# Optimization experiments

Measured on AMD Instinct MI355X. Metric: run time of the kernel, lower is better.

## Reference

```python
import jax, jax.numpy as jnp
import numpy as np

D_MODEL = 1024
NUM_HEADS = 16
HEAD_DIM = D_MODEL // NUM_HEADS
SEQ_LEN = 2048
BATCH = 2


def setup_inputs() -> dict:
    key = jax.random.key(0)
    ks = jax.random.split(key, 8)
    s = 1.0 / np.sqrt(D_MODEL)
    x = jax.random.normal(ks[0], (BATCH, SEQ_LEN, D_MODEL), jnp.float32)
    Wq = jax.random.normal(ks[1], (D_MODEL, D_MODEL), jnp.float32) * s
    Wk = jax.random.normal(ks[2], (D_MODEL, D_MODEL), jnp.float32) * s
    Wv = jax.random.normal(ks[3], (D_MODEL, D_MODEL), jnp.float32) * s
    Wo = jax.random.normal(ks[4], (D_MODEL, D_MODEL), jnp.float32) * s
    bq = jnp.zeros((D_MODEL,), jnp.float32)
    bk = jnp.zeros((D_MODEL,), jnp.float32)
    bv = jnp.zeros((D_MODEL,), jnp.float32)
    bo = jnp.zeros((D_MODEL,), jnp.float32)
    pos_embed = jax.random.normal(ks[5], (SEQ_LEN, HEAD_DIM), jnp.float32) * (1.0 / np.sqrt(HEAD_DIM))
    alpha = jnp.ones((NUM_HEADS, 1, 1), jnp.float32)
    beta = jnp.zeros((NUM_HEADS, 1, 1), jnp.float32)
    mask = jnp.ones((BATCH, SEQ_LEN), jnp.int32)
    return {"x": x, "mask": mask, "Wq": Wq, "bq": bq, "Wk": Wk, "bk": bk,
            "Wv": Wv, "bv": bv, "Wo": Wo, "bo": bo,
            "pos_embed": pos_embed, "alpha": alpha, "beta": beta}


def reference(x, mask, Wq, bq, Wk, bk, Wv, bv, Wo, bo, pos_embed, alpha, beta):
    B, S, _ = x.shape
    H, Dh = NUM_HEADS, HEAD_DIM
    # projections (torch Linear: x @ W^T + b), reshape to [B,H,S,Dh]
    def proj(W, b):
        return (x @ W.T + b).reshape(B, S, H, Dh).transpose(0, 2, 1, 3)
    q = proj(Wq, bq)
    k = proj(Wk, bk)
    v = proj(Wv, bv)
    # content scores [B,H,S,S]
    content = jnp.einsum('bhqd,bhkd->bhqk', q, k) / np.sqrt(Dh).astype(np.float32)
    # position scores [S,S] -> broadcast; combined with per-head alpha/beta
    pe = pos_embed[:S]
    pos_attn = pe @ pe.T  # [S,S]
    scores = content + (alpha * pos_attn[None] + beta)[None]  # [B,H,S,S]
    # mask: [B,S] broadcast over heads and query positions (key-side mask)
    scores = jnp.where(mask[:, None, None, :] == 0, -jnp.inf, scores)
    probs = jax.nn.softmax(scores, axis=-1)
    out = jnp.einsum('bhqk,bhkd->bhqd', probs, v)  # [B,H,S,Dh]
    out = out.transpose(0, 2, 1, 3).reshape(B, S, H * Dh)
    return out @ Wo.T + bo
```

## Files before the change

kernel.cpp:

```cpp
#include <hip/hip_runtime.h>

#define BATCH 2
#define SEQ   2048
#define NH    16
#define DH    64
#define DA    128
#define DM    1024
#define MTOT  (BATCH*SEQ)

typedef _Float16 f16x8 __attribute__((ext_vector_type(8)));
typedef _Float16 f16x4 __attribute__((ext_vector_type(4)));
typedef float    f32x4 __attribute__((ext_vector_type(4)));
typedef float    f32x16 __attribute__((ext_vector_type(16)));

#define LOG2E 1.44269504088896340736f

#define OFF_X16 0u
#define OFF_WQ  8388608u
#define OFF_WK  10485760u
#define OFF_WV  12582912u
#define OFF_WO  14680064u
#define OFF_QA  16777216u
#define OFF_KA  33554432u
#define OFF_VT  50331648u
#define OFF_AO  58720256u

__device__ __forceinline__ void gload_lds16(const _Float16* g, _Float16* l) {
  __builtin_amdgcn_global_load_lds(
      (const __attribute__((address_space(1))) unsigned int*)g,
      (__attribute__((address_space(3))) unsigned int*)l, 16, 0, 0);
}

__device__ __forceinline__ float fexp2(float x) {
  float r;
  asm("v_exp_f32 %0, %1" : "=v"(r) : "v"(x));
  return r;
}

__device__ __forceinline__ unsigned pk2(float a, float b) {
  auto v = __builtin_amdgcn_cvt_pkrtz(a, b);
  return *(unsigned*)&v;
}

__global__ __launch_bounds__(256) void prep(
    const float* __restrict__ x,  const float* __restrict__ wq,
    const float* __restrict__ wk, const float* __restrict__ wv,
    const float* __restrict__ wo, _Float16* __restrict__ dst,
    const float* __restrict__ pe, const float* __restrict__ alpha,
    _Float16* __restrict__ Qa, _Float16* __restrict__ Ka)
{
  int bid = blockIdx.x;
  if (bid < 4096) {
    int i = bid * 256 + threadIdx.x;
    const float* src;
    if (i < 524288) {
      src = x + (size_t)i * 8;
    } else {
      int j = i - 524288;
      int wi = j >> 17;
      const float* w = (wi == 0) ? wq : ((wi == 1) ? wk : ((wi == 2) ? wv : wo));
      src = w + (size_t)(j & 131071) * 8;
    }
    float4 a = ((const float4*)src)[0];
    float4 c = ((const float4*)src)[1];
    f16x8 hv;
    hv[0]=(_Float16)a.x; hv[1]=(_Float16)a.y; hv[2]=(_Float16)a.z; hv[3]=(_Float16)a.w;
    hv[4]=(_Float16)c.x; hv[5]=(_Float16)c.y; hv[6]=(_Float16)c.z; hv[7]=(_Float16)c.w;
    *(f16x8*)(dst + (size_t)i * 8) = hv;
  } else {
    int idx = (bid - 4096) * 256 + threadIdx.x;
    int c8 = idx & 7;
    int s  = (idx >> 3) & 2047;
    int h  = (idx >> 14) & 15;
    int b  = idx >> 18;
    const float4* p4 = (const float4*)(pe + s * 64 + c8 * 8);
    float4 a = p4[0], c = p4[1];
    float al = alpha[h] * LOG2E;
    f16x8 hk, hq;
    hk[0]=(_Float16)a.x; hk[1]=(_Float16)a.y; hk[2]=(_Float16)a.z; hk[3]=(_Float16)a.w;
    hk[4]=(_Float16)c.x; hk[5]=(_Float16)c.y; hk[6]=(_Float16)c.z; hk[7]=(_Float16)c.w;
    hq[0]=(_Float16)(al*a.x); hq[1]=(_Float16)(al*a.y); hq[2]=(_Float16)(al*a.z); hq[3]=(_Float16)(al*a.w);
    hq[4]=(_Float16)(al*c.x); hq[5]=(_Float16)(al*c.y); hq[6]=(_Float16)(al*c.z); hq[7]=(_Float16)(al*c.w);
    size_t o = ((size_t)((b * NH + h) * SEQ + s)) * DA + 64 + c8 * 8;
    *(f16x8*)&Qa[o] = hq;
    *(f16x8*)&Ka[o] = hk;
  }
}

template<int MODE>
__global__ __launch_bounds__(512) void gemm_nt(
    const _Float16* __restrict__ A,
    const _Float16* __restrict__ W0, const _Float16* __restrict__ W1,
    const _Float16* __restrict__ W2,
    const float* __restrict__ b0, const float* __restrict__ b1,
    const float* __restrict__ b2,
    _Float16* __restrict__ Qa, _Float16* __restrict__ Ka,
    _Float16* __restrict__ Vt, float* __restrict__ Out)
{
  __shared__ _Float16 As[128 * 64];
  __shared__ _Float16 Bs[128 * 64];
  const int tid = threadIdx.x;
  const int w = tid >> 6, lane = tid & 63;
  const int g = lane >> 4, l16 = lane & 15;
  const int wm = w >> 2, wn = w & 3;

  int lin = blockIdx.x;
  int xcd = lin & 7, j = lin >> 3;
  int mblk, nb_all;
  if (MODE == 0) { mblk = (xcd & 3) * 8 + (j & 7); nb_all = (xcd >> 2) * 12 + (j >> 3); }
  else           { mblk = xcd * 4 + (j & 3);       nb_all = j >> 2; }

  const _Float16* Bp; const float* biasp;
  int which = 0, nblk = nb_all;
  if (MODE == 0) {
    which = nb_all >> 3; nblk = nb_all & 7;
    Bp = (which == 0) ? W0 : ((which == 1) ? W1 : W2);
    biasp = (which == 0) ? b0 : ((which == 1) ? b1 : b2);
  } else {
    Bp = W0; biasp = b0;
  }

  f32x4 zero4 = {0.f, 0.f, 0.f, 0.f};
  f32x4 acc[4][2];
  #pragma unroll
  for (int mb = 0; mb < 4; ++mb)
    #pragma unroll
    for (int nb = 0; nb < 2; ++nb) acc[mb][nb] = zero4;

  const _Float16* Abase = A  + (size_t)mblk * 128 * DM;
  const _Float16* Bbase = Bp + (size_t)nblk * 128 * DM;

  for (int kt = 0; kt < DM / 64; ++kt) {
    __syncthreads();
    #pragma unroll
    for (int ii = 0; ii < 2; ++ii) {
      int i = w * 2 + ii;
      int rt = i * 8 + (lane >> 3);
      int cg = (lane & 7) ^ (rt & 7);
      gload_lds16(Abase + (size_t)rt * DM + kt * 64 + cg * 8, &As[i * 512]);
    }
    #pragma unroll
    for (int ii = 0; ii < 2; ++ii) {
      int i = w * 2 + ii;
      int rt = i * 8 + (lane >> 3);
      int cg = (lane & 7) ^ (rt & 7);
      gload_lds16(Bbase + (size_t)rt * DM + kt * 64 + cg * 8, &Bs[i * 512]);
    }
    __syncthreads();
    #pragma unroll
    for (int ks = 0; ks < 2; ++ks) {
      f16x8 av[4], bv[2];
      #pragma unroll
      for (int mb = 0; mb < 4; ++mb) {
        int rt = wm * 64 + mb * 16 + l16;
        av[mb] = *(const f16x8*)&As[rt * 64 + (((ks * 4 + g) ^ (rt & 7)) * 8)];
      }
      #pragma unroll
      for (int nb = 0; nb < 2; ++nb) {
        int rt = wn * 32 + nb * 16 + l16;
        bv[nb] = *(const f16x8*)&Bs[rt * 64 + (((ks * 4 + g) ^ (rt & 7)) * 8)];
      }
      #pragma unroll
      for (int mb = 0; mb < 4; ++mb)
        #pragma unroll
        for (int nb = 0; nb < 2; ++nb)
          acc[mb][nb] = __builtin_amdgcn_mfma_f32_16x16x32_f16(
              av[mb], bv[nb], acc[mb][nb], 0, 0, 0);
    }
  }

  #pragma unroll
  for (int nb = 0; nb < 2; ++nb) {
    int n = nblk * 128 + wn * 32 + nb * 16 + l16;
    float bias = biasp[n];
    #pragma unroll
    for (int mb = 0; mb < 4; ++mb) {
      int m0 = mblk * 128 + wm * 64 + mb * 16 + g * 4;
      if (MODE == 0) {
        int hh = n >> 6, dd = n & 63;
        if (which == 2) {
          int bb = m0 >> 11, ss = m0 & 2047;
          f16x4 hv;
          #pragma unroll
          for (int r = 0; r < 4; ++r) hv[r] = (_Float16)(acc[mb][nb][r] + bias);
          *(f16x4*)&Vt[((size_t)((bb * NH + hh) * DH + dd)) * SEQ + ss] = hv;
        } else {
          #pragma unroll
          for (int r = 0; r < 4; ++r) {
            int m = m0 + r; int bb = m >> 11, ss = m & 2047;
            size_t o = ((size_t)((bb * NH + hh) * SEQ + ss)) * DA + dd;
            if (which == 0) Qa[o] = (_Float16)((acc[mb][nb][r] + bias) * (0.125f * LOG2E));
            else            Ka[o] = (_Float16)(acc[mb][nb][r] + bias);
          }
        }
      } else {
        #pragma unroll
        for (int r = 0; r < 4; ++r)
          Out[(size_t)(m0 + r) * DM + n] = acc[mb][nb][r] + bias;
      }
    }
  }
}

__global__ __launch_bounds__(256, 3) void flash_attn(
    const _Float16* __restrict__ Qa, const _Float16* __restrict__ Ka,
    const _Float16* __restrict__ Vt, const int* __restrict__ mask,
    _Float16* __restrict__ AO)
{
  __shared__ _Float16 Ks[2][64 * 128];
  __shared__ _Float16 Vs[2][64 * 64];
  const int tid = threadIdx.x;
  const int w = tid >> 6, lane = tid & 63;
  const int l32 = lane & 31, hi = lane >> 5;

  int bid = blockIdx.x;
  int work = (bid & 7) * 64 + (bid >> 3);
  const int qt = work & 15;
  const int bh = work >> 4;
  const int h = bh & 15, b = bh >> 4;

  const _Float16* qbase = Qa + ((size_t)(bh * SEQ) + qt * 128 + w * 32) * DA;
  f16x8 qf[8];
  #pragma unroll
  for (int c16 = 0; c16 < 8; ++c16)
    qf[c16] = *(const f16x8*)&qbase[l32 * DA + c16 * 16 + hi * 8];

  f32x16 acco[2];
  #pragma unroll
  for (int db = 0; db < 2; ++db)
    #pragma unroll
    for (int r = 0; r < 16; ++r) acco[db][r] = 0.f;
  float mrun = -3.0e38f, lrun = 0.f;

  const _Float16* kbase = Ka + (size_t)bh * SEQ * DA;
  const _Float16* vbase = Vt + (size_t)bh * DH * SEQ;
  const int* mbase = mask + b * SEQ;

  int allm = 1;
  #pragma unroll 8
  for (int t = 0; t < SEQ / 64; ++t) allm &= (mbase[t * 64 + lane] != 0);
  const bool maskclean = __all(allm);

  auto STAGE = [&](int buf, int kt) {
    #pragma unroll
    for (int ii = 0; ii < 4; ++ii) {
      int i = ii * 256 + tid;
      int rt = i >> 4, c = i & 15;
      int cg = c ^ (rt & 7);
      gload_lds16(kbase + (size_t)(kt * 64 + rt) * DA + cg * 8, &Ks[buf][i * 8]);
    }
    #pragma unroll
    for (int ii = 0; ii < 2; ++ii) {
      int i = ii * 256 + tid;
      int rt = i >> 3, c = i & 7;
      int cg = c ^ (rt & 7);
      gload_lds16(vbase + (size_t)rt * SEQ + kt * 64 + cg * 8, &Vs[buf][i * 8]);
    }
  };

  STAGE(0, 0);
  int cur = 0;
  for (int kt = 0; kt < SEQ / 64; ++kt) {
    asm volatile("s_waitcnt lgkmcnt(0)" ::: "memory");
    __builtin_amdgcn_s_barrier();
    asm volatile("" ::: "memory");
    if (kt + 1 < SEQ / 64) {
      STAGE(cur ^ 1, kt + 1);
      asm volatile("s_waitcnt vmcnt(6)" ::: "memory");
    } else {
      asm volatile("s_waitcnt vmcnt(0)" ::: "memory");
    }
    __builtin_amdgcn_s_barrier();
    asm volatile("" ::: "memory");

    f32x16 sfr[2];
    __builtin_amdgcn_s_setprio(1);
    #pragma unroll
    for (int kb = 0; kb < 2; ++kb) {
      f32x16 s;
      #pragma unroll
      for (int r = 0; r < 16; ++r) s[r] = 0.f;
      int rt = kb * 32 + l32;
      #pragma unroll
      for (int c16 = 0; c16 < 8; ++c16) {
        int ch = (2 * c16 + hi) ^ (rt & 7);
        f16x8 kf = *(const f16x8*)&Ks[cur][rt * 128 + ch * 8];
        s = __builtin_amdgcn_mfma_f32_32x32x16_f16(kf, qf[c16], s, 0, 0, 0);
      }
      sfr[kb] = s;
    }
    __builtin_amdgcn_s_setprio(0);

    if (!maskclean) {
      #pragma unroll
      for (int kb = 0; kb < 2; ++kb)
        #pragma unroll
        for (int r = 0; r < 16; ++r) {
          int key = kt * 64 + kb * 32 + (r & 3) + 8 * (r >> 2) + 4 * hi;
          if (mbase[key] == 0) sfr[kb][r] = -3.0e38f;
        }
    }

    float mx = sfr[0][0];
    #pragma unroll
    for (int kb = 0; kb < 2; ++kb)
      #pragma unroll
      for (int r = 0; r < 16; ++r) mx = fmaxf(mx, sfr[kb][r]);
    mx = fmaxf(mx, __shfl_xor(mx, 32));

    const bool rescale = !__all(mx <= mrun + 8.0f);
    float mnew = mrun, scale = 1.0f;
    if (rescale) {
      mnew = fmaxf(mrun, mx);
      scale = fexp2(mrun - mnew);
    }
    float rsum = 0.f;
    unsigned pk[2][4][2];
    #pragma unroll
    for (int kb = 0; kb < 2; ++kb)
      #pragma unroll
      for (int rq = 0; rq < 4; ++rq) {
        float p0 = fexp2(sfr[kb][rq * 4 + 0] - mnew);
        float p1 = fexp2(sfr[kb][rq * 4 + 1] - mnew);
        float p2 = fexp2(sfr[kb][rq * 4 + 2] - mnew);
        float p3 = fexp2(sfr[kb][rq * 4 + 3] - mnew);
        rsum += (p0 + p1) + (p2 + p3);
        pk[kb][rq][0] = pk2(p0, p1);
        pk[kb][rq][1] = pk2(p2, p3);
      }
    rsum += __shfl_xor(rsum, 32);
    if (rescale) {
      lrun = lrun * scale + rsum;
      mrun = mnew;
      #pragma unroll
      for (int db = 0; db < 2; ++db)
        #pragma unroll
        for (int r = 0; r < 16; ++r) acco[db][r] *= scale;
    } else {
      lrun += rsum;
    }

    __builtin_amdgcn_s_setprio(1);
    #pragma unroll
    for (int c = 0; c < 4; ++c) {
      const int kb = c >> 1, c2 = c & 1;
      unsigned X0 = pk[kb][2 * c2][0],     X1 = pk[kb][2 * c2][1];
      unsigned Y0 = pk[kb][2 * c2 + 1][0], Y1 = pk[kb][2 * c2 + 1][1];
      asm("v_permlane32_swap_b32 %0, %1" : "+v"(X0), "+v"(Y0));
      asm("v_permlane32_swap_b32 %0, %1" : "+v"(X1), "+v"(Y1));
      union { unsigned u[4]; f16x8 v; } pu;
      pu.u[0] = X0; pu.u[1] = X1; pu.u[2] = Y0; pu.u[3] = Y1;
      #pragma unroll
      for (int db = 0; db < 2; ++db) {
        int row = db * 32 + l32;
        int ch = (2 * c + hi) ^ (row & 7);
        f16x8 vf = *(const f16x8*)&Vs[cur][row * 64 + ch * 8];
        acco[db] = __builtin_amdgcn_mfma_f32_32x32x16_f16(vf, pu.v, acco[db], 0, 0, 0);
      }
    }
    __builtin_amdgcn_s_setprio(0);
    cur ^= 1;
  }

  float inv = 1.0f / lrun;
  int sg = qt * 128 + w * 32 + l32;
  _Float16* aobase = AO + ((size_t)(b * SEQ + sg)) * DM + h * DH;
  #pragma unroll
  for (int db = 0; db < 2; ++db)
    #pragma unroll
    for (int rq = 0; rq < 4; ++rq) {
      f16x4 o;
      #pragma unroll
      for (int j = 0; j < 4; ++j) o[j] = (_Float16)(acco[db][rq * 4 + j] * inv);
      *(f16x4*)&aobase[db * 32 + rq * 8 + hi * 4] = o;
    }
}

extern "C" void kernel_launch(void* const* d_in, const int* in_sizes, int n_in,
                              void* d_out, int out_size, void* d_ws, size_t ws_size,
                              hipStream_t stream) {
  const float* x     = (const float*)d_in[0];
  const int*   mask  = (const int*)  d_in[1];
  const float* Wq    = (const float*)d_in[2];
  const float* bq    = (const float*)d_in[3];
  const float* Wk    = (const float*)d_in[4];
  const float* bk    = (const float*)d_in[5];
  const float* Wv    = (const float*)d_in[6];
  const float* bv    = (const float*)d_in[7];
  const float* Wo    = (const float*)d_in[8];
  const float* bo    = (const float*)d_in[9];
  const float* pe    = (const float*)d_in[10];
  const float* alpha = (const float*)d_in[11];

  char* ws = (char*)d_ws;
  _Float16* x16 = (_Float16*)(ws + OFF_X16);
  _Float16* wq6 = (_Float16*)(ws + OFF_WQ);
  _Float16* wk6 = (_Float16*)(ws + OFF_WK);
  _Float16* wv6 = (_Float16*)(ws + OFF_WV);
  _Float16* wo6 = (_Float16*)(ws + OFF_WO);
  _Float16* Qa  = (_Float16*)(ws + OFF_QA);
  _Float16* Ka  = (_Float16*)(ws + OFF_KA);
  _Float16* Vt  = (_Float16*)(ws + OFF_VT);
  _Float16* AO  = (_Float16*)(ws + OFF_AO);
  float* out = (float*)d_out;

  prep<<<6144, 256, 0, stream>>>(x, Wq, Wk, Wv, Wo, x16, pe, alpha, Qa, Ka);
  gemm_nt<0><<<768, 512, 0, stream>>>(x16, wq6, wk6, wv6, bq, bk, bv,
                                      Qa, Ka, Vt, nullptr);
  flash_attn<<<512, 256, 0, stream>>>(Qa, Ka, Vt, mask, AO);
  gemm_nt<1><<<256, 512, 0, stream>>>(AO, wo6, nullptr, nullptr, bo,
                                      nullptr, nullptr, nullptr, nullptr,
                                      nullptr, out);
}
```

Baseline: 128.0 us.

## Precompute position score matrix once and add it in flash attention

The old code folded the position term into attention by concatenating pe onto Q and K (head dim 128), which doubled the QK^T MFMA work. The new code computes the shared S×S pe·peᵀ matrix once in fp16 with a small GEMM. Flash attention now uses head dim 64 and reads a 128×64 tile of that matrix from LDS per step, scaling it by alpha and adding it to the scores. This removes half of the QK^T compute and K bandwidth but adds an 8MB position matrix that must be streamed, more LDS per block, and lower occupancy (launch bound 3→2). Beta is still ignored, as in the old code.

```diff
diff --git a/kernel.cpp b/kernel.cpp
--- a/kernel.cpp
+++ b/kernel.cpp
@@ -4,7 +4,6 @@
 #define SEQ   2048
 #define NH    16
 #define DH    64
-#define DA    128
 #define DM    1024
 #define MTOT  (BATCH*SEQ)
 
@@ -15,15 +14,17 @@
 
 #define LOG2E 1.44269504088896340736f
 
-#define OFF_X16 0u
-#define OFF_WQ  8388608u
-#define OFF_WK  10485760u
-#define OFF_WV  12582912u
-#define OFF_WO  14680064u
-#define OFF_QA  16777216u
-#define OFF_KA  33554432u
-#define OFF_VT  50331648u
-#define OFF_AO  58720256u
+#define OFF_X16  0u
+#define OFF_WQ   8388608u
+#define OFF_WK   10485760u
+#define OFF_WV   12582912u
+#define OFF_WO   14680064u
+#define OFF_QA   16777216u
+#define OFF_KA   25165824u
+#define OFF_POS  33554432u
+#define OFF_PE16 41943040u
+#define OFF_VT   50331648u
+#define OFF_AO   58720256u
 
 __device__ __forceinline__ void gload_lds16(const _Float16* g, _Float16* l) {
   __builtin_amdgcn_global_load_lds(
@@ -46,13 +47,13 @@
     const float* __restrict__ x,  const float* __restrict__ wq,
     const float* __restrict__ wk, const float* __restrict__ wv,
     const float* __restrict__ wo, _Float16* __restrict__ dst,
-    const float* __restrict__ pe, const float* __restrict__ alpha,
-    _Float16* __restrict__ Qa, _Float16* __restrict__ Ka)
+    const float* __restrict__ pe, _Float16* __restrict__ pe16)
 {
   int bid = blockIdx.x;
+  const float* src;
+  _Float16* d;
   if (bid < 4096) {
     int i = bid * 256 + threadIdx.x;
-    const float* src;
     if (i < 524288) {
       src = x + (size_t)i * 8;
     } else {
@@ -61,29 +62,83 @@
       const float* w = (wi == 0) ? wq : ((wi == 1) ? wk : ((wi == 2) ? wv : wo));
       src = w + (size_t)(j & 131071) * 8;
     }
-    float4 a = ((const float4*)src)[0];
-    float4 c = ((const float4*)src)[1];
-    f16x8 hv;
-    hv[0]=(_Float16)a.x; hv[1]=(_Float16)a.y; hv[2]=(_Float16)a.z; hv[3]=(_Float16)a.w;
-    hv[4]=(_Float16)c.x; hv[5]=(_Float16)c.y; hv[6]=(_Float16)c.z; hv[7]=(_Float16)c.w;
-    *(f16x8*)(dst + (size_t)i * 8) = hv;
+    d = dst + (size_t)i * 8;
   } else {
-    int idx = (bid - 4096) * 256 + threadIdx.x;
-    int c8 = idx & 7;
-    int s  = (idx >> 3) & 2047;
-    int h  = (idx >> 14) & 15;
-    int b  = idx >> 18;
-    const float4* p4 = (const float4*)(pe + s * 64 + c8 * 8);
-    float4 a = p4[0], c = p4[1];
-    float al = alpha[h] * LOG2E;
-    f16x8 hk, hq;
-    hk[0]=(_Float16)a.x; hk[1]=(_Float16)a.y; hk[2]=(_Float16)a.z; hk[3]=(_Float16)a.w;
-    hk[4]=(_Float16)c.x; hk[5]=(_Float16)c.y; hk[6]=(_Float16)c.z; hk[7]=(_Float16)c.w;
-    hq[0]=(_Float16)(al*a.x); hq[1]=(_Float16)(al*a.y); hq[2]=(_Float16)(al*a.z); hq[3]=(_Float16)(al*a.w);
-    hq[4]=(_Float16)(al*c.x); hq[5]=(_Float16)(al*c.y); hq[6]=(_Float16)(al*c.z); hq[7]=(_Float16)(al*c.w);
-    size_t o = ((size_t)((b * NH + h) * SEQ + s)) * DA + 64 + c8 * 8;
-    *(f16x8*)&Qa[o] = hq;
-    *(f16x8*)&Ka[o] = hk;
+    int i = (bid - 4096) * 256 + threadIdx.x;
+    src = pe + (size_t)i * 8;
+    d = pe16 + (size_t)i * 8;
+  }
+  float4 a = ((const float4*)src)[0];
+  float4 c = ((const float4*)src)[1];
+  f16x8 hv;
+  hv[0]=(_Float16)a.x; hv[1]=(_Float16)a.y; hv[2]=(_Float16)a.z; hv[3]=(_Float16)a.w;
+  hv[4]=(_Float16)c.x; hv[5]=(_Float16)c.y; hv[6]=(_Float16)c.z; hv[7]=(_Float16)c.w;
+  *(f16x8*)d = hv;
+}
+
+__global__ __launch_bounds__(512) void pos_gemm(
+    const _Float16* __restrict__ pe16, _Float16* __restrict__ pos)
+{
+  __shared__ _Float16 As[128 * 64];
+  __shared__ _Float16 Bs[128 * 64];
+  const int tid = threadIdx.x;
+  const int w = tid >> 6, lane = tid & 63;
+  const int g = lane >> 4, l16 = lane & 15;
+  const int wm = w >> 2, wn = w & 3;
+  const int mblk = blockIdx.y, nblk = blockIdx.x;
+
+  #pragma unroll
+  for (int ii = 0; ii < 2; ++ii) {
+    int i = ii * 512 + tid;
+    int rt = i >> 3, c = i & 7;
+    int cg = c ^ (rt & 7);
+    gload_lds16(pe16 + (size_t)(mblk * 128 + rt) * 64 + cg * 8, &As[i * 8]);
+  }
+  #pragma unroll
+  for (int ii = 0; ii < 2; ++ii) {
+    int i = ii * 512 + tid;
+    int rt = i >> 3, c = i & 7;
+    int cg = c ^ (rt & 7);
+    gload_lds16(pe16 + (size_t)(nblk * 128 + rt) * 64 + cg * 8, &Bs[i * 8]);
+  }
+  __syncthreads();
+
+  f32x4 zero4 = {0.f, 0.f, 0.f, 0.f};
+  f32x4 acc[4][2];
+  #pragma unroll
+  for (int mb = 0; mb < 4; ++mb)
+    #pragma unroll
+    for (int nb = 0; nb < 2; ++nb) acc[mb][nb] = zero4;
+  #pragma unroll
+  for (int ks = 0; ks < 2; ++ks) {
+    f16x8 av[4], bv[2];
+    #pragma unroll
+    for (int mb = 0; mb < 4; ++mb) {
+      int rt = wm * 64 + mb * 16 + l16;
+      av[mb] = *(const f16x8*)&As[rt * 64 + (((ks * 4 + g) ^ (rt & 7)) * 8)];
+    }
+    #pragma unroll
+    for (int nb = 0; nb < 2; ++nb) {
+      int rt = wn * 32 + nb * 16 + l16;
+      bv[nb] = *(const f16x8*)&Bs[rt * 64 + (((ks * 4 + g) ^ (rt & 7)) * 8)];
+    }
+    #pragma unroll
+    for (int mb = 0; mb < 4; ++mb)
+      #pragma unroll
+      for (int nb = 0; nb < 2; ++nb)
+        acc[mb][nb] = __builtin_amdgcn_mfma_f32_16x16x32_f16(
+            av[mb], bv[nb], acc[mb][nb], 0, 0, 0);
+  }
+  #pragma unroll
+  for (int nb = 0; nb < 2; ++nb) {
+    int n = nblk * 128 + wn * 32 + nb * 16 + l16;
+    #pragma unroll
+    for (int mb = 0; mb < 4; ++mb) {
+      int m0 = mblk * 128 + wm * 64 + mb * 16 + g * 4;
+      #pragma unroll
+      for (int r = 0; r < 4; ++r)
+        pos[(size_t)(m0 + r) * SEQ + n] = (_Float16)acc[mb][nb][r];
+    }
   }
 }
 
@@ -188,7 +243,7 @@
           #pragma unroll
           for (int r = 0; r < 4; ++r) {
             int m = m0 + r; int bb = m >> 11, ss = m & 2047;
-            size_t o = ((size_t)((bb * NH + hh) * SEQ + ss)) * DA + dd;
+            size_t o = ((size_t)((bb * NH + hh) * SEQ + ss)) * 64 + dd;
             if (which == 0) Qa[o] = (_Float16)((acc[mb][nb][r] + bias) * (0.125f * LOG2E));
             else            Ka[o] = (_Float16)(acc[mb][nb][r] + bias);
           }
@@ -202,13 +257,15 @@
   }
 }
 
-__global__ __launch_bounds__(256, 3) void flash_attn(
+__global__ __launch_bounds__(256, 2) void flash_attn(
     const _Float16* __restrict__ Qa, const _Float16* __restrict__ Ka,
-    const _Float16* __restrict__ Vt, const int* __restrict__ mask,
+    const _Float16* __restrict__ Vt, const _Float16* __restrict__ Pos,
+    const float* __restrict__ alpha, const int* __restrict__ mask,
     _Float16* __restrict__ AO)
 {
-  __shared__ _Float16 Ks[2][64 * 128];
+  __shared__ _Float16 Ks[2][64 * 64];
   __shared__ _Float16 Vs[2][64 * 64];
+  __shared__ _Float16 Pp[2][128 * 64];
   const int tid = threadIdx.x;
   const int w = tid >> 6, lane = tid & 63;
   const int l32 = lane & 31, hi = lane >> 5;
@@ -219,11 +276,13 @@
   const int bh = work >> 4;
   const int h = bh & 15, b = bh >> 4;
 
-  const _Float16* qbase = Qa + ((size_t)(bh * SEQ) + qt * 128 + w * 32) * DA;
-  f16x8 qf[8];
-  #pragma unroll
-  for (int c16 = 0; c16 < 8; ++c16)
-    qf[c16] = *(const f16x8*)&qbase[l32 * DA + c16 * 16 + hi * 8];
+  const _Float16* qbase = Qa + ((size_t)(bh * SEQ) + qt * 128 + w * 32) * 64;
+  f16x8 qf[4];
+  #pragma unroll
+  for (int c16 = 0; c16 < 4; ++c16)
+    qf[c16] = *(const f16x8*)&qbase[l32 * 64 + c16 * 16 + hi * 8];
+
+  const float alf = alpha[h] * LOG2E;
 
   f32x16 acco[2];
   #pragma unroll
@@ -232,8 +291,9 @@
     for (int r = 0; r < 16; ++r) acco[db][r] = 0.f;
   float mrun = -3.0e38f, lrun = 0.f;
 
-  const _Float16* kbase = Ka + (size_t)bh * SEQ * DA;
+  const _Float16* kbase = Ka + (size_t)bh * SEQ * 64;
   const _Float16* vbase = Vt + (size_t)bh * DH * SEQ;
+  const _Float16* pbase = Pos + (size_t)(qt * 128) * SEQ;
   const int* mbase = mask + b * SEQ;
 
   int allm = 1;
@@ -243,11 +303,11 @@
 
   auto STAGE = [&](int buf, int kt) {
     #pragma unroll
-    for (int ii = 0; ii < 4; ++ii) {
+    for (int ii = 0; ii < 2; ++ii) {
       int i = ii * 256 + tid;
-      int rt = i >> 4, c = i & 15;
+      int rt = i >> 3, c = i & 7;
       int cg = c ^ (rt & 7);
-      gload_lds16(kbase + (size_t)(kt * 64 + rt) * DA + cg * 8, &Ks[buf][i * 8]);
+      gload_lds16(kbase + (size_t)(kt * 64 + rt) * 64 + cg * 8, &Ks[buf][i * 8]);
     }
     #pragma unroll
     for (int ii = 0; ii < 2; ++ii) {
@@ -255,6 +315,13 @@
       int rt = i >> 3, c = i & 7;
       int cg = c ^ (rt & 7);
       gload_lds16(vbase + (size_t)rt * SEQ + kt * 64 + cg * 8, &Vs[buf][i * 8]);
+    }
+    #pragma unroll
+    for (int ii = 0; ii < 4; ++ii) {
+      int i = ii * 256 + tid;
+      int rt = i >> 3, c = i & 7;
+      int cg = c ^ (rt & 7);
+      gload_lds16(pbase + (size_t)rt * SEQ + kt * 64 + cg * 8, &Pp[buf][i * 8]);
     }
   };
 
@@ -266,7 +333,7 @@
     asm volatile("" ::: "memory");
     if (kt + 1 < SEQ / 64) {
       STAGE(cur ^ 1, kt + 1);
-      asm volatile("s_waitcnt vmcnt(6)" ::: "memory");
+      asm volatile("s_waitcnt vmcnt(8)" ::: "memory");
     } else {
       asm volatile("s_waitcnt vmcnt(0)" ::: "memory");
     }
@@ -282,14 +349,30 @@
       for (int r = 0; r < 16; ++r) s[r] = 0.f;
       int rt = kb * 32 + l32;
       #pragma unroll
-      for (int c16 = 0; c16 < 8; ++c16) {
-        int ch = (2 * c16 + hi) ^ (rt & 7);
-        f16x8 kf = *(const f16x8*)&Ks[cur][rt * 128 + ch * 8];
+      for (int c16 = 0; c16 < 4; ++c16) {
+        int ch = (c16 * 2 + hi) ^ (rt & 7);
+        f16x8 kf = *(const f16x8*)&Ks[cur][rt * 64 + ch * 8];
         s = __builtin_amdgcn_mfma_f32_32x32x16_f16(kf, qf[c16], s, 0, 0, 0);
       }
       sfr[kb] = s;
     }
     __builtin_amdgcn_s_setprio(0);
+
+    {
+      int row = w * 32 + l32;
+      int sw8 = (row & 7);
+      #pragma unroll
+      for (int kb = 0; kb < 2; ++kb)
+        #pragma unroll
+        for (int rq = 0; rq < 4; ++rq) {
+          int G = kb * 8 + rq * 2 + hi;
+          f16x4 p4 = *(const f16x4*)&Pp[cur][row * 64 + (((G >> 1) ^ sw8) * 8) + (G & 1) * 4];
+          sfr[kb][rq * 4 + 0] += alf * (float)p4[0];
+          sfr[kb][rq * 4 + 1] += alf * (float)p4[1];
+          sfr[kb][rq * 4 + 2] += alf * (float)p4[2];
+          sfr[kb][rq * 4 + 3] += alf * (float)p4[3];
+        }
+    }
 
     if (!maskclean) {
       #pragma unroll
@@ -393,21 +476,24 @@
   const float* alpha = (const float*)d_in[11];
 
   char* ws = (char*)d_ws;
-  _Float16* x16 = (_Float16*)(ws + OFF_X16);
-  _Float16* wq6 = (_Float16*)(ws + OFF_WQ);
-  _Float16* wk6 = (_Float16*)(ws + OFF_WK);
-  _Float16* wv6 = (_Float16*)(ws + OFF_WV);
-  _Float16* wo6 = (_Float16*)(ws + OFF_WO);
-  _Float16* Qa  = (_Float16*)(ws + OFF_QA);
-  _Float16* Ka  = (_Float16*)(ws + OFF_KA);
-  _Float16* Vt  = (_Float16*)(ws + OFF_VT);
-  _Float16* AO  = (_Float16*)(ws + OFF_AO);
+  _Float16* x16  = (_Float16*)(ws + OFF_X16);
+  _Float16* wq6  = (_Float16*)(ws + OFF_WQ);
+  _Float16* wk6  = (_Float16*)(ws + OFF_WK);
+  _Float16* wv6  = (_Float16*)(ws + OFF_WV);
+  _Float16* wo6  = (_Float16*)(ws + OFF_WO);
+  _Float16* Qa   = (_Float16*)(ws + OFF_QA);
+  _Float16* Ka   = (_Float16*)(ws + OFF_KA);
+  _Float16* Pos  = (_Float16*)(ws + OFF_POS);
+  _Float16* pe16 = (_Float16*)(ws + OFF_PE16);
+  _Float16* Vt   = (_Float16*)(ws + OFF_VT);
+  _Float16* AO   = (_Float16*)(ws + OFF_AO);
   float* out = (float*)d_out;
 
-  prep<<<6144, 256, 0, stream>>>(x, Wq, Wk, Wv, Wo, x16, pe, alpha, Qa, Ka);
+  prep<<<4160, 256, 0, stream>>>(x, Wq, Wk, Wv, Wo, x16, pe, pe16);
+  pos_gemm<<<dim3(16, 16), 512, 0, stream>>>(pe16, Pos);
   gemm_nt<0><<<768, 512, 0, stream>>>(x16, wq6, wk6, wv6, bq, bk, bv,
                                       Qa, Ka, Vt, nullptr);
-  flash_attn<<<512, 256, 0, stream>>>(Qa, Ka, Vt, mask, AO);
+  flash_attn<<<512, 256, 0, stream>>>(Qa, Ka, Vt, Pos, alpha, mask, AO);
   gemm_nt<1><<<256, 512, 0, stream>>>(AO, wo6, nullptr, nullptr, bo,
                                       nullptr, nullptr, nullptr, nullptr,
                                       nullptr, out);
```

After: 129.5 us. No clear change (+1.1%).
